# Kernel tuning notes

Measured on AMD Instinct MI355X. Metric: run time of the kernel, lower is better.

## Reference

```python
import jax, jax.numpy as jnp
import numpy as np

B, N, D, E, H = 8, 128, 64, 3, 256
L = E + 1  # edge label 0 = 'no edge' (dropped by edge_types[:, 1:])
DEC_OUT = 64


def setup_inputs() -> dict:
    key = jax.random.key(0)
    ks = jax.random.split(key, 8)
    node_states = jax.random.normal(ks[0], (B, 1, N, D), dtype=jnp.float32)
    # one-hot edge-type labels [B, N, N, L]
    type_ids = jax.random.randint(ks[1], (B, N, N), 0, L)
    edges = jax.nn.one_hot(type_ids, L, dtype=jnp.float32)
    def lin(k, fan_in, shape):
        return jax.random.normal(k, shape, dtype=jnp.float32) / jnp.sqrt(jnp.float32(fan_in))
    return {
        "node_states": node_states,
        "edges": edges,
        # per-edge-type encoder MLP (2 layers, relu after each)
        "We1": lin(ks[2], 2 * D, (E, 2 * D, H)),
        "be1": jnp.zeros((E, H), dtype=jnp.float32),
        "We2": lin(ks[3], H, (E, H, H)),
        "be2": jnp.zeros((E, H), dtype=jnp.float32),
        # node decoder MLP (2 layers, relu after each)
        "Wd1": lin(ks[4], D + H, (D + H, H)),
        "bd1": jnp.zeros((H,), dtype=jnp.float32),
        "Wd2": lin(ks[5], H, (H, DEC_OUT)),
        "bd2": jnp.zeros((DEC_OUT,), dtype=jnp.float32),
    }


def reference(node_states, edges, We1, be1, We2, be2, Wd1, bd1, Wd2, bd2):
    b, _, n, d = node_states.shape
    ns = node_states[:, 0]  # [B, N, D]
    # NodePropagator: for fully-connected edges, the one-hot matmuls are a
    # gather: edge e = (i, j) gets [ns[i], ns[j]] (flat index i*N + j).
    msg_src = jnp.broadcast_to(ns[:, :, None, :], (b, n, n, d))  # source i
    msg_tgt = jnp.broadcast_to(ns[:, None, :, :], (b, n, n, d))  # target j
    node_msgs = jnp.concatenate([msg_src, msg_tgt], -1).reshape(b, n * n, 2 * d)
    # EdgeEncoder: one 2-layer relu MLP per edge type -> [B, E, N^2, H]
    h = jax.nn.relu(jnp.einsum("bmd,edh->bemh", node_msgs, We1) + be1[None, :, None, :])
    h = jax.nn.relu(jnp.einsum("bemh,ehk->bemk", h, We2) + be2[None, :, None, :])
    # mask by edge-type indicator; type 0 (no edge) is dropped
    edge_types = jnp.transpose(edges.reshape(b, n * n, L), (0, 2, 1))  # [B, L, N^2]
    edge_msgs = h * edge_types[:, 1:, :, None]  # [B, E, N^2, H]
    # EdgeAggregator: edge_targets^T matmul = scatter-sum over sources i per
    # target j, then sum over edge types (dim 1, keepdim).
    aggr = edge_msgs.reshape(b, E, n, n, H).sum(axis=2)  # [B, E, N, H]
    aggr = aggr.sum(axis=1, keepdims=True)  # [B, 1, N, H]
    # node decoder
    dec_in = jnp.concatenate([node_states, aggr], -1)  # [B, 1, N, D+H]
    out = jax.nn.relu(dec_in @ Wd1 + bd1)
    out = jax.nn.relu(out @ Wd2 + bd2)
    return out  # [B, 1, N, DEC_OUT]
```

## Files before the change

kernel.cpp:

```cpp
#include <hip/hip_runtime.h>

#define NB 8
#define NN 128
#define ND 64
#define NE 3
#define NH 256
#define NOUT 64

typedef short bf16x8_t __attribute__((ext_vector_type(8)));
typedef float f32x4_t __attribute__((ext_vector_type(4)));
typedef unsigned short ushort_t;

static __device__ __forceinline__ unsigned short f2bf(float f) {
    unsigned u = __float_as_uint(f);
    u += 0x7FFFu + ((u >> 16) & 1u);
    return (unsigned short)(u >> 16);
}
static __device__ __forceinline__ unsigned pk2bf(float a, float b) {
    return (unsigned)f2bf(a) | ((unsigned)f2bf(b) << 16);
}

static __device__ __forceinline__ bf16x8_t a_genf(float4 p0, float4 p1, float4 q0, float4 q1) {
    union { uint4 u; bf16x8_t v; } r;
    r.u.x = pk2bf(fmaxf(p0.x + q0.x, 0.f), fmaxf(p0.y + q0.y, 0.f));
    r.u.y = pk2bf(fmaxf(p0.z + q0.z, 0.f), fmaxf(p0.w + q0.w, 0.f));
    r.u.z = pk2bf(fmaxf(p1.x + q1.x, 0.f), fmaxf(p1.y + q1.y, 0.f));
    r.u.w = pk2bf(fmaxf(p1.z + q1.z, 0.f), fmaxf(p1.w + q1.w, 0.f));
    return r.v;
}

#define IT 16
__global__ __launch_bounds__(256) void prep_kernel(
    const float* __restrict__ We2, const float* __restrict__ ns,
    const float* __restrict__ We1, const float* __restrict__ be1,
    const float* __restrict__ edges,
    ushort_t* __restrict__ We2p,
    float* __restrict__ P, float* __restrict__ Q,
    ushort_t* __restrict__ list_ws, int4* __restrict__ cnts_ws)
{
    const int t = threadIdx.x;
    const int blk = blockIdx.x;

    if (blk < 48) {
        __shared__ float slab[256][16];
        const int e = blk >> 4, nfg = blk & 15;
        const int n0 = nfg * 16;
#pragma unroll
        for (int it = 0; it < 16; it++) {
            const int k = (t >> 4) + it * 16;
            slab[k][t & 15] = We2[((size_t)e * NH + k) * NH + n0 + (t & 15)];
        }
        __syncthreads();
        ushort_t* dst = We2p + ((size_t)e * 16 + nfg) * 4096;
#pragma unroll
        for (int it = 0; it < 16; it++) {
            const int idx = it * 256 + t;
            const int kk = idx >> 9;
            const int ln = (idx >> 3) & 63;
            const int jj = idx & 7;
            const int k = kk * 32 + (ln >> 4) * 8 + jj;
            dst[idx] = f2bf(slab[k][ln & 15]);
        }
        return;
    }
    if (blk < 240) {
        __shared__ float ns_lds[IT][ND];
        const int blk2 = blk - 48;
        const int itile = blk2 & 7;
        const int e = (blk2 >> 3) % NE;
        const int b = blk2 / 24;
        const int i0 = itile * IT;
        for (int x = t; x < IT * ND; x += 256)
            ns_lds[x / ND][x % ND] = ns[(size_t)(b * NN + i0 + x / ND) * ND + (x % ND)];
        __syncthreads();
        const int h = t;
        float accP[IT], accQ[IT];
        const float bias = be1[e * NH + h];
#pragma unroll
        for (int m = 0; m < IT; m++) { accP[m] = 0.f; accQ[m] = bias; }
        const float* W1 = We1 + (size_t)e * 2 * ND * NH + h;
        for (int d = 0; d < ND; d++) {
            const float w1 = W1[(size_t)d * NH];
            const float w2 = W1[(size_t)(ND + d) * NH];
#pragma unroll
            for (int m = 0; m < IT; m++) {
                accP[m] = fmaf(ns_lds[m][d], w1, accP[m]);
                accQ[m] = fmaf(ns_lds[m][d], w2, accQ[m]);
            }
        }
#pragma unroll
        for (int m = 0; m < IT; m++) {
            const size_t idx = ((size_t)((b * NE + e) * NN) + i0 + m) * NH + h;
            P[idx] = accP[m];
            Q[idx] = accQ[m];
        }
        return;
    }
    {
        __shared__ unsigned long long wm[2][NE];
        const int pb = blk - 240;
        const int b = pb >> 7, j = pb & 127;
        const int lane = t & 63, wave = t >> 6;
        int ecls = -1;
        if (t < 128) {
            const float4 ev = *(const float4*)(edges + ((size_t)(b * NN + t) * NN + j) * 4);
            ecls = ev.y > 0.5f ? 0 : (ev.z > 0.5f ? 1 : (ev.w > 0.5f ? 2 : -1));
#pragma unroll
            for (int ee = 0; ee < NE; ee++) {
                unsigned long long m = __ballot(ecls == ee);
                if (lane == 0) wm[wave][ee] = m;
            }
        }
        __syncthreads();
        const int c0 = __popcll(wm[0][0]) + __popcll(wm[1][0]);
        const int c1 = __popcll(wm[0][1]) + __popcll(wm[1][1]);
        const int c2 = __popcll(wm[0][2]) + __popcll(wm[1][2]);
        if (t < 128 && ecls >= 0) {
            const unsigned long long lower = (1ull << lane) - 1ull;
            int pos = __popcll(wm[wave][ecls] & lower);
            if (wave == 1) pos += __popcll(wm[0][ecls]);
            pos += (ecls > 0 ? c0 : 0) + (ecls > 1 ? c1 : 0);
            list_ws[(size_t)pb * NN + pos] = (ushort_t)t;
        }
        if (t == 0) { int4 cc; cc.x = c0; cc.y = c1; cc.z = c2; cc.w = 0; cnts_ws[pb] = cc; }
    }
}

__global__ __launch_bounds__(1024) void gemm_kernel(
    const float* __restrict__ Pf,
    const float* __restrict__ Qf,
    const ushort_t* __restrict__ We2p,
    const float* __restrict__ be2,
    const ushort_t* __restrict__ list_ws,
    const int4* __restrict__ cnts_ws,
    float* __restrict__ aggr3)
{
    const int blk = blockIdx.x;
    const int jh = blk & 7;
    const int e  = (blk >> 3) % 3;
    const int b  = blk / 24;
    const int tid = threadIdx.x;
    const int lane = tid & 63;
    const int wave = tid >> 6;

    __shared__ __align__(16) ushort_t Bl[16 * 8 * 512];

    {
        const ushort_t* Bsrc = We2p + (size_t)e * 65536;
#pragma unroll
        for (int it = 0; it < 8; it++) {
            const int o = it * 8192 + tid * 8;
            *(uint4*)&Bl[o] = *(const uint4*)&Bsrc[o];
        }
    }

    const int j = jh * 16 + wave;
    const int4 cc = cnts_ws[b * NN + j];
    const int ce = e == 0 ? cc.x : (e == 1 ? cc.y : cc.z);
    const int start = (e > 0 ? cc.x : 0) + (e > 1 ? cc.y : 0);
    const ushort_t* Lj = list_ws + (size_t)(b * NN + j) * NN + start;
    const float* Qj = Qf + (size_t)((b * NE + e) * NN + j) * NH;
    const float* Pb = Pf + (size_t)(b * NE + e) * NN * NH;

    float bb[16];
#pragma unroll
    for (int nf = 0; nf < 16; nf++)
        bb[nf] = be2[e * NH + nf * 16 + (lane & 15)];

    __syncthreads();

    float rsum[16];
#pragma unroll
    for (int nf = 0; nf < 16; nf++) rsum[nf] = 0.f;

    if (ce > 0) {
        const int F = (ce + 15) >> 4;
        for (int f = 0; f < F; f++) {
            int p = f * 16 + (lane & 15);
            p = p < ce ? p : ce - 1;
            const float* P0 = Pb + (size_t)Lj[p] * NH;

            f32x4_t acc[16];
            const f32x4_t z4 = {0.f, 0.f, 0.f, 0.f};
#pragma unroll
            for (int nf = 0; nf < 16; nf++) acc[nf] = z4;

#pragma unroll 2
            for (int kk = 0; kk < 8; kk++) {
                const int ko = kk * 32 + (lane >> 4) * 8;
                const float4 q0 = *(const float4*)(Qj + ko);
                const float4 q1 = *(const float4*)(Qj + ko + 4);
                const float4 p0 = *(const float4*)(P0 + ko);
                const float4 p1 = *(const float4*)(P0 + ko + 4);
                const bf16x8_t af = a_genf(p0, p1, q0, q1);
#pragma unroll
                for (int nf = 0; nf < 16; nf++) {
                    const bf16x8_t bfr = *(const bf16x8_t*)(&Bl[(nf * 8 + kk) * 512 + lane * 8]);
                    acc[nf] = __builtin_amdgcn_mfma_f32_16x16x32_bf16(af, bfr, acc[nf], 0, 0, 0);
                }
            }
#pragma unroll
            for (int nf = 0; nf < 16; nf++) {
                float s = 0.f;
#pragma unroll
                for (int r = 0; r < 4; r++) {
                    const int pos = f * 16 + ((lane >> 4) << 2) + r;
                    if (pos < ce) s += fmaxf(acc[nf][r] + bb[nf], 0.f);
                }
                s += __shfl_xor(s, 16, 64);
                s += __shfl_xor(s, 32, 64);
                if (lane < 16) rsum[nf] += s;
            }
        }
    }
    if (lane < 16) {
        float* dst = aggr3 + (size_t)((b * NE + e) * NN + j) * NH + lane;
#pragma unroll
        for (int nf = 0; nf < 16; nf++) dst[nf * 16] = rsum[nf];
    }
}

__global__ __launch_bounds__(256) void dec_kernel(
    const float* __restrict__ ns,
    const float* __restrict__ aggr3,
    const float* __restrict__ Wd1, const float* __restrict__ bd1,
    const float* __restrict__ Wd2, const float* __restrict__ bd2,
    float* __restrict__ out)
{
    const int b = blockIdx.x >> 5;
    const int jq = blockIdx.x & 31;
    const int tid = threadIdx.x;
    __shared__ __align__(16) float xs[4][320];
    __shared__ __align__(16) float o1s[4][NH];

    for (int x = tid; x < 4 * 320; x += 256) {
        const int jj = x / 320, k = x % 320;
        const int j = jq * 4 + jj;
        float v;
        if (k < ND) v = ns[(size_t)(b * NN + j) * ND + k];
        else {
            const int c = k - ND;
            v = aggr3[(size_t)((b * NE + 0) * NN + j) * NH + c]
              + aggr3[(size_t)((b * NE + 1) * NN + j) * NH + c]
              + aggr3[(size_t)((b * NE + 2) * NN + j) * NH + c];
        }
        xs[jj][k] = v;
    }
    __syncthreads();
    {
        const int n = tid;
        float acc[4];
        const float b1 = bd1[n];
#pragma unroll
        for (int jj = 0; jj < 4; jj++) acc[jj] = b1;
        for (int k4 = 0; k4 < 80; k4++) {
            const float w0 = Wd1[(size_t)(k4 * 4 + 0) * NH + n];
            const float w1 = Wd1[(size_t)(k4 * 4 + 1) * NH + n];
            const float w2 = Wd1[(size_t)(k4 * 4 + 2) * NH + n];
            const float w3 = Wd1[(size_t)(k4 * 4 + 3) * NH + n];
#pragma unroll
            for (int jj = 0; jj < 4; jj++) {
                const float4 xv = *(const float4*)(&xs[jj][k4 * 4]);
                acc[jj] = fmaf(xv.x, w0, fmaf(xv.y, w1, fmaf(xv.z, w2, fmaf(xv.w, w3, acc[jj]))));
            }
        }
#pragma unroll
        for (int jj = 0; jj < 4; jj++) o1s[jj][n] = fmaxf(acc[jj], 0.f);
    }
    __syncthreads();
    {
        const int jj = tid >> 6, col = tid & 63;
        float a = bd2[col];
        for (int h4 = 0; h4 < 64; h4++) {
            const float4 ov = *(const float4*)(&o1s[jj][h4 * 4]);
            a = fmaf(ov.x, Wd2[(size_t)(h4 * 4 + 0) * NOUT + col], a);
            a = fmaf(ov.y, Wd2[(size_t)(h4 * 4 + 1) * NOUT + col], a);
            a = fmaf(ov.z, Wd2[(size_t)(h4 * 4 + 2) * NOUT + col], a);
            a = fmaf(ov.w, Wd2[(size_t)(h4 * 4 + 3) * NOUT + col], a);
        }
        const int j = jq * 4 + jj;
        out[(size_t)(b * NN + j) * NOUT + col] = fmaxf(a, 0.f);
    }
}

extern "C" void kernel_launch(void* const* d_in, const int* in_sizes, int n_in,
                              void* d_out, int out_size, void* d_ws, size_t ws_size,
                              hipStream_t stream)
{
    const float* ns    = (const float*)d_in[0];
    const float* edges = (const float*)d_in[1];
    const float* We1   = (const float*)d_in[2];
    const float* be1   = (const float*)d_in[3];
    const float* We2   = (const float*)d_in[4];
    const float* be2   = (const float*)d_in[5];
    const float* Wd1   = (const float*)d_in[6];
    const float* bd1   = (const float*)d_in[7];
    const float* Wd2   = (const float*)d_in[8];
    const float* bd2   = (const float*)d_in[9];
    float* outp = (float*)d_out;

    float* Pf = (float*)d_ws;
    float* Qf = Pf + (size_t)NB * NE * NN * NH;
    ushort_t* We2p = (ushort_t*)(Qf + (size_t)NB * NE * NN * NH);
    ushort_t* list_ws = We2p + (size_t)NE * NH * NH;
    int4* cnts_ws = (int4*)(list_ws + (size_t)NB * NN * NN);
    float* aggr3 = (float*)(cnts_ws + NB * NN);

    hipLaunchKernelGGL(prep_kernel, dim3(1264), dim3(256), 0, stream,
                       We2, ns, We1, be1, edges, We2p, Pf, Qf, list_ws, cnts_ws);
    hipLaunchKernelGGL(gemm_kernel, dim3(192), dim3(1024), 0, stream,
                       Pf, Qf, We2p, be2, list_ws, cnts_ws, aggr3);
    hipLaunchKernelGGL(dec_kernel, dim3(256), dim3(256), 0, stream,
                       ns, aggr3, Wd1, bd1, Wd2, bd2, outp);
}
```

Baseline: 80.69 us.

## Fuse edge-list build, per-type edge GEMM and node decoder into one kernel

Moves the per-target edge-type list construction out of the prep kernel and into a new fused kernel. That kernel also runs the edge MLP second layer over all three edge types and then the node decoder for 4 target nodes per 1024-thread block. It drops the aggr3 and list/count workspace round trips and one kernel launch. In exchange, each block reloads the We2 tile into LDS three times, each wave handles only 64 output columns, and the grid shrinks to 256 blocks with serialized loops over edge types.

```diff
diff --git a/kernel.cpp b/kernel.cpp
--- a/kernel.cpp
+++ b/kernel.cpp
@@ -33,10 +33,8 @@
 __global__ __launch_bounds__(256) void prep_kernel(
     const float* __restrict__ We2, const float* __restrict__ ns,
     const float* __restrict__ We1, const float* __restrict__ be1,
-    const float* __restrict__ edges,
     ushort_t* __restrict__ We2p,
-    float* __restrict__ P, float* __restrict__ Q,
-    ushort_t* __restrict__ list_ws, int4* __restrict__ cnts_ws)
+    float* __restrict__ P, float* __restrict__ Q)
 {
     const int t = threadIdx.x;
     const int blk = blockIdx.x;
@@ -63,7 +61,7 @@
         }
         return;
     }
-    if (blk < 240) {
+    {
         __shared__ float ns_lds[IT][ND];
         const int blk2 = blk - 48;
         const int itile = blk2 & 7;
@@ -94,192 +92,167 @@
             P[idx] = accP[m];
             Q[idx] = accQ[m];
         }
-        return;
-    }
-    {
-        __shared__ unsigned long long wm[2][NE];
-        const int pb = blk - 240;
-        const int b = pb >> 7, j = pb & 127;
-        const int lane = t & 63, wave = t >> 6;
-        int ecls = -1;
-        if (t < 128) {
-            const float4 ev = *(const float4*)(edges + ((size_t)(b * NN + t) * NN + j) * 4);
-            ecls = ev.y > 0.5f ? 0 : (ev.z > 0.5f ? 1 : (ev.w > 0.5f ? 2 : -1));
-#pragma unroll
-            for (int ee = 0; ee < NE; ee++) {
-                unsigned long long m = __ballot(ecls == ee);
-                if (lane == 0) wm[wave][ee] = m;
-            }
-        }
-        __syncthreads();
-        const int c0 = __popcll(wm[0][0]) + __popcll(wm[1][0]);
-        const int c1 = __popcll(wm[0][1]) + __popcll(wm[1][1]);
-        const int c2 = __popcll(wm[0][2]) + __popcll(wm[1][2]);
-        if (t < 128 && ecls >= 0) {
-            const unsigned long long lower = (1ull << lane) - 1ull;
-            int pos = __popcll(wm[wave][ecls] & lower);
-            if (wave == 1) pos += __popcll(wm[0][ecls]);
-            pos += (ecls > 0 ? c0 : 0) + (ecls > 1 ? c1 : 0);
-            list_ws[(size_t)pb * NN + pos] = (ushort_t)t;
-        }
-        if (t == 0) { int4 cc; cc.x = c0; cc.y = c1; cc.z = c2; cc.w = 0; cnts_ws[pb] = cc; }
-    }
-}
-
-__global__ __launch_bounds__(1024) void gemm_kernel(
+    }
+}
+
+__global__ __launch_bounds__(1024) void fused_kernel(
+    const float* __restrict__ ns,
+    const float* __restrict__ edges,
     const float* __restrict__ Pf,
     const float* __restrict__ Qf,
     const ushort_t* __restrict__ We2p,
     const float* __restrict__ be2,
-    const ushort_t* __restrict__ list_ws,
-    const int4* __restrict__ cnts_ws,
-    float* __restrict__ aggr3)
-{
-    const int blk = blockIdx.x;
-    const int jh = blk & 7;
-    const int e  = (blk >> 3) % 3;
-    const int b  = blk / 24;
-    const int tid = threadIdx.x;
-    const int lane = tid & 63;
-    const int wave = tid >> 6;
-
-    __shared__ __align__(16) ushort_t Bl[16 * 8 * 512];
-
-    {
-        const ushort_t* Bsrc = We2p + (size_t)e * 65536;
-#pragma unroll
-        for (int it = 0; it < 8; it++) {
-            const int o = it * 8192 + tid * 8;
-            *(uint4*)&Bl[o] = *(const uint4*)&Bsrc[o];
-        }
-    }
-
-    const int j = jh * 16 + wave;
-    const int4 cc = cnts_ws[b * NN + j];
-    const int ce = e == 0 ? cc.x : (e == 1 ? cc.y : cc.z);
-    const int start = (e > 0 ? cc.x : 0) + (e > 1 ? cc.y : 0);
-    const ushort_t* Lj = list_ws + (size_t)(b * NN + j) * NN + start;
-    const float* Qj = Qf + (size_t)((b * NE + e) * NN + j) * NH;
-    const float* Pb = Pf + (size_t)(b * NE + e) * NN * NH;
-
-    float bb[16];
-#pragma unroll
-    for (int nf = 0; nf < 16; nf++)
-        bb[nf] = be2[e * NH + nf * 16 + (lane & 15)];
-
-    __syncthreads();
-
-    float rsum[16];
-#pragma unroll
-    for (int nf = 0; nf < 16; nf++) rsum[nf] = 0.f;
-
-    if (ce > 0) {
-        const int F = (ce + 15) >> 4;
-        for (int f = 0; f < F; f++) {
-            int p = f * 16 + (lane & 15);
-            p = p < ce ? p : ce - 1;
-            const float* P0 = Pb + (size_t)Lj[p] * NH;
-
-            f32x4_t acc[16];
-            const f32x4_t z4 = {0.f, 0.f, 0.f, 0.f};
-#pragma unroll
-            for (int nf = 0; nf < 16; nf++) acc[nf] = z4;
-
-#pragma unroll 2
-            for (int kk = 0; kk < 8; kk++) {
-                const int ko = kk * 32 + (lane >> 4) * 8;
-                const float4 q0 = *(const float4*)(Qj + ko);
-                const float4 q1 = *(const float4*)(Qj + ko + 4);
-                const float4 p0 = *(const float4*)(P0 + ko);
-                const float4 p1 = *(const float4*)(P0 + ko + 4);
-                const bf16x8_t af = a_genf(p0, p1, q0, q1);
-#pragma unroll
-                for (int nf = 0; nf < 16; nf++) {
-                    const bf16x8_t bfr = *(const bf16x8_t*)(&Bl[(nf * 8 + kk) * 512 + lane * 8]);
-                    acc[nf] = __builtin_amdgcn_mfma_f32_16x16x32_bf16(af, bfr, acc[nf], 0, 0, 0);
-                }
-            }
-#pragma unroll
-            for (int nf = 0; nf < 16; nf++) {
-                float s = 0.f;
-#pragma unroll
-                for (int r = 0; r < 4; r++) {
-                    const int pos = f * 16 + ((lane >> 4) << 2) + r;
-                    if (pos < ce) s += fmaxf(acc[nf][r] + bb[nf], 0.f);
-                }
-                s += __shfl_xor(s, 16, 64);
-                s += __shfl_xor(s, 32, 64);
-                if (lane < 16) rsum[nf] += s;
-            }
-        }
-    }
-    if (lane < 16) {
-        float* dst = aggr3 + (size_t)((b * NE + e) * NN + j) * NH + lane;
-#pragma unroll
-        for (int nf = 0; nf < 16; nf++) dst[nf * 16] = rsum[nf];
-    }
-}
-
-__global__ __launch_bounds__(256) void dec_kernel(
-    const float* __restrict__ ns,
-    const float* __restrict__ aggr3,
     const float* __restrict__ Wd1, const float* __restrict__ bd1,
     const float* __restrict__ Wd2, const float* __restrict__ bd2,
     float* __restrict__ out)
 {
     const int b = blockIdx.x >> 5;
     const int jq = blockIdx.x & 31;
+    const int j0 = jq * 4;
     const int tid = threadIdx.x;
+    const int lane = tid & 63;
+    const int wave = tid >> 6;
+    const int jj = wave >> 2;
+    const int cq = wave & 3;
+    const int j = j0 + jj;
+
+    __shared__ __align__(16) ushort_t Bl[16 * 8 * 512];
+    __shared__ ushort_t lists[4][NN];
+    __shared__ int cnts[4][3];
+    __shared__ unsigned long long wm[4][2][3];
+    __shared__ float aggrL[4][NH];
     __shared__ __align__(16) float xs[4][320];
     __shared__ __align__(16) float o1s[4][NH];
 
-    for (int x = tid; x < 4 * 320; x += 256) {
-        const int jj = x / 320, k = x % 320;
-        const int j = jq * 4 + jj;
-        float v;
-        if (k < ND) v = ns[(size_t)(b * NN + j) * ND + k];
-        else {
-            const int c = k - ND;
-            v = aggr3[(size_t)((b * NE + 0) * NN + j) * NH + c]
-              + aggr3[(size_t)((b * NE + 1) * NN + j) * NH + c]
-              + aggr3[(size_t)((b * NE + 2) * NN + j) * NH + c];
-        }
-        xs[jj][k] = v;
+    int ecls = -1;
+    if (tid < 512) {
+        const int ii = tid & 127;
+        const float4 ev = *(const float4*)(edges + ((size_t)(b * NN + ii) * NN + j0 + (tid >> 7)) * 4);
+        ecls = ev.y > 0.5f ? 0 : (ev.z > 0.5f ? 1 : (ev.w > 0.5f ? 2 : -1));
+    }
+#pragma unroll
+    for (int ee = 0; ee < 3; ee++) {
+        unsigned long long m = __ballot(ecls == ee);
+        if (lane == 0 && wave < 8) wm[wave >> 1][wave & 1][ee] = m;
+    }
+    __syncthreads();
+    if (tid < 512 && ecls >= 0) {
+        const int jl = tid >> 7, w2 = (tid >> 6) & 1, ii = tid & 127;
+        const unsigned long long lower = (1ull << lane) - 1ull;
+        int pos = __popcll(wm[jl][w2][ecls] & lower);
+        if (w2) pos += __popcll(wm[jl][0][ecls]);
+        const int c0 = __popcll(wm[jl][0][0]) + __popcll(wm[jl][1][0]);
+        const int c1 = __popcll(wm[jl][0][1]) + __popcll(wm[jl][1][1]);
+        pos += (ecls > 0 ? c0 : 0) + (ecls > 1 ? c1 : 0);
+        lists[jl][pos] = (ushort_t)ii;
+    }
+    if (tid < 16) {
+        const int jl = tid >> 2, ee = tid & 3;
+        if (ee < 3) cnts[jl][ee] = __popcll(wm[jl][0][ee]) + __popcll(wm[jl][1][ee]);
+    }
+
+    float rsum[4] = {0.f, 0.f, 0.f, 0.f};
+
+    for (int e = 0; e < NE; e++) {
+        __syncthreads();
+        {
+            const ushort_t* Bsrc = We2p + (size_t)e * 65536;
+#pragma unroll
+            for (int it = 0; it < 8; it++) {
+                const int o = it * 8192 + tid * 8;
+                *(uint4*)&Bl[o] = *(const uint4*)&Bsrc[o];
+            }
+        }
+        __syncthreads();
+
+        const int ce = cnts[jj][e];
+        const int start = (e > 0 ? cnts[jj][0] : 0) + (e > 1 ? cnts[jj][1] : 0);
+        const ushort_t* Lj = &lists[jj][start];
+        const float* Qj = Qf + (size_t)((b * NE + e) * NN + j) * NH;
+        const float* Pb = Pf + (size_t)(b * NE + e) * NN * NH;
+        float bb[4];
+#pragma unroll
+        for (int nf = 0; nf < 4; nf++)
+            bb[nf] = be2[e * NH + cq * 64 + nf * 16 + (lane & 15)];
+
+        if (ce > 0) {
+            const int F = (ce + 15) >> 4;
+            for (int f = 0; f < F; f++) {
+                int p = f * 16 + (lane & 15);
+                p = p < ce ? p : ce - 1;
+                const float* P0 = Pb + (size_t)Lj[p] * NH;
+
+                f32x4_t acc[4];
+                const f32x4_t z4 = {0.f, 0.f, 0.f, 0.f};
+#pragma unroll
+                for (int nf = 0; nf < 4; nf++) acc[nf] = z4;
+
+#pragma unroll 2
+                for (int kk = 0; kk < 8; kk++) {
+                    const int ko = kk * 32 + (lane >> 4) * 8;
+                    const float4 q0 = *(const float4*)(Qj + ko);
+                    const float4 q1 = *(const float4*)(Qj + ko + 4);
+                    const float4 p0 = *(const float4*)(P0 + ko);
+                    const float4 p1 = *(const float4*)(P0 + ko + 4);
+                    const bf16x8_t af = a_genf(p0, p1, q0, q1);
+#pragma unroll
+                    for (int nf = 0; nf < 4; nf++) {
+                        const bf16x8_t bfr = *(const bf16x8_t*)(&Bl[((cq * 4 + nf) * 8 + kk) * 512 + lane * 8]);
+                        acc[nf] = __builtin_amdgcn_mfma_f32_16x16x32_bf16(af, bfr, acc[nf], 0, 0, 0);
+                    }
+                }
+#pragma unroll
+                for (int nf = 0; nf < 4; nf++) {
+                    float s = 0.f;
+#pragma unroll
+                    for (int r = 0; r < 4; r++) {
+                        const int pos = f * 16 + ((lane >> 4) << 2) + r;
+                        if (pos < ce) s += fmaxf(acc[nf][r] + bb[nf], 0.f);
+                    }
+                    s += __shfl_xor(s, 16, 64);
+                    s += __shfl_xor(s, 32, 64);
+                    if (lane < 16) rsum[nf] += s;
+                }
+            }
+        }
+    }
+
+    if (lane < 16) {
+#pragma unroll
+        for (int nf = 0; nf < 4; nf++)
+            aggrL[jj][cq * 64 + nf * 16 + lane] = rsum[nf];
+    }
+    __syncthreads();
+
+    for (int x = tid; x < 4 * 320; x += 1024) {
+        const int jl = x / 320, k = x % 320;
+        xs[jl][k] = k < ND ? ns[(size_t)(b * NN + j0 + jl) * ND + k] : aggrL[jl][k - ND];
     }
     __syncthreads();
     {
-        const int n = tid;
-        float acc[4];
-        const float b1 = bd1[n];
-#pragma unroll
-        for (int jj = 0; jj < 4; jj++) acc[jj] = b1;
+        const int jl = tid >> 8, n = tid & 255;
+        float a = bd1[n];
         for (int k4 = 0; k4 < 80; k4++) {
-            const float w0 = Wd1[(size_t)(k4 * 4 + 0) * NH + n];
-            const float w1 = Wd1[(size_t)(k4 * 4 + 1) * NH + n];
-            const float w2 = Wd1[(size_t)(k4 * 4 + 2) * NH + n];
-            const float w3 = Wd1[(size_t)(k4 * 4 + 3) * NH + n];
-#pragma unroll
-            for (int jj = 0; jj < 4; jj++) {
-                const float4 xv = *(const float4*)(&xs[jj][k4 * 4]);
-                acc[jj] = fmaf(xv.x, w0, fmaf(xv.y, w1, fmaf(xv.z, w2, fmaf(xv.w, w3, acc[jj]))));
-            }
-        }
-#pragma unroll
-        for (int jj = 0; jj < 4; jj++) o1s[jj][n] = fmaxf(acc[jj], 0.f);
-    }
-    __syncthreads();
-    {
-        const int jj = tid >> 6, col = tid & 63;
+            const float4 xv = *(const float4*)(&xs[jl][k4 * 4]);
+            a = fmaf(xv.x, Wd1[(size_t)(k4 * 4 + 0) * NH + n], a);
+            a = fmaf(xv.y, Wd1[(size_t)(k4 * 4 + 1) * NH + n], a);
+            a = fmaf(xv.z, Wd1[(size_t)(k4 * 4 + 2) * NH + n], a);
+            a = fmaf(xv.w, Wd1[(size_t)(k4 * 4 + 3) * NH + n], a);
+        }
+        o1s[jl][n] = fmaxf(a, 0.f);
+    }
+    __syncthreads();
+    if (tid < 256) {
+        const int jl = tid >> 6, col = tid & 63;
         float a = bd2[col];
         for (int h4 = 0; h4 < 64; h4++) {
-            const float4 ov = *(const float4*)(&o1s[jj][h4 * 4]);
+            const float4 ov = *(const float4*)(&o1s[jl][h4 * 4]);
             a = fmaf(ov.x, Wd2[(size_t)(h4 * 4 + 0) * NOUT + col], a);
             a = fmaf(ov.y, Wd2[(size_t)(h4 * 4 + 1) * NOUT + col], a);
             a = fmaf(ov.z, Wd2[(size_t)(h4 * 4 + 2) * NOUT + col], a);
             a = fmaf(ov.w, Wd2[(size_t)(h4 * 4 + 3) * NOUT + col], a);
         }
-        const int j = jq * 4 + jj;
-        out[(size_t)(b * NN + j) * NOUT + col] = fmaxf(a, 0.f);
+        out[(size_t)(b * NN + j0 + jl) * NOUT + col] = fmaxf(a, 0.f);
     }
 }
 
@@ -302,14 +275,9 @@
     float* Pf = (float*)d_ws;
     float* Qf = Pf + (size_t)NB * NE * NN * NH;
     ushort_t* We2p = (ushort_t*)(Qf + (size_t)NB * NE * NN * NH);
-    ushort_t* list_ws = We2p + (size_t)NE * NH * NH;
-    int4* cnts_ws = (int4*)(list_ws + (size_t)NB * NN * NN);
-    float* aggr3 = (float*)(cnts_ws + NB * NN);
-
-    hipLaunchKernelGGL(prep_kernel, dim3(1264), dim3(256), 0, stream,
-                       We2, ns, We1, be1, edges, We2p, Pf, Qf, list_ws, cnts_ws);
-    hipLaunchKernelGGL(gemm_kernel, dim3(192), dim3(1024), 0, stream,
-                       Pf, Qf, We2p, be2, list_ws, cnts_ws, aggr3);
-    hipLaunchKernelGGL(dec_kernel, dim3(256), dim3(256), 0, stream,
-                       ns, aggr3, Wd1, bd1, Wd2, bd2, outp);
-}
+
+    hipLaunchKernelGGL(prep_kernel, dim3(240), dim3(256), 0, stream,
+                       We2, ns, We1, be1, We2p, Pf, Qf);
+    hipLaunchKernelGGL(fused_kernel, dim3(256), dim3(1024), 0, stream,
+                       ns, edges, Pf, Qf, We2p, be2, Wd1, bd1, Wd2, bd2, outp);
+}
```

Measured after the change: 108.8 us. 34.9% more time.
